# Kernel optimization log

Hardware: AMD Instinct MI355X
Metric: run time of the kernel (lower is better)

Reference implementation:

```python
import jax, jax.numpy as jnp
import numpy as np

M = 16            # num_frequencies
DIM = 512         # dim_input
B = 32768         # flattened batch
H = M + 1         # raw complex table side
N = 2 * M + 1     # autocorrelated table side
NPAR = H * H      # (m+1)^2


def setup_inputs() -> dict:
    key = jax.random.key(0)
    k1, k2, k3 = jax.random.split(key, 3)
    inputs = jax.random.normal(k1, (B, DIM), dtype=jnp.float32)
    targets = jax.random.uniform(k2, (B, 2), dtype=jnp.float32)  # points in [0,1) subset of [-1,1]^2
    # nn.init.normal_(weight, 0.01) => mean=0.01, std=1.0 ; bias zeros
    W = jax.random.normal(k3, (2 * NPAR, DIM), dtype=jnp.float32) + 0.01
    b = jnp.zeros((2 * NPAR,), dtype=jnp.float32)
    return {"inputs": inputs, "targets": targets, "W": W, "b": b}


def reference(inputs, targets, W, b):
    # Linear -> unconstrained complex (m+1)x(m+1) table per sample
    p = inputs @ W.T + b                                   # (B, 2*NPAR)
    real = p[:, :NPAR].reshape(-1, H, H)
    imag = p[:, NPAR:].reshape(-1, H, H)
    seq = jax.lax.complex(real, imag)                      # (B, H, H) complex64

    # 2D linear autocorrelation r[tau] = sum_i seq[i+tau] * conj(seq[i]),
    # tau in [-M, M]^2, via zero-padded FFT (equivalent to the grouped conv2d).
    F = jnp.fft.fft2(seq, s=(N, N))                        # (B, N, N)
    ac = jnp.fft.ifft2(F * jnp.conj(F))                    # circular autocorr
    ac = jnp.roll(ac, (M, M), axis=(-2, -1))               # index a -> lag a-M

    # Normalize so C[0,0] (= centre) equals 1/4 => unit mass on [-1,1]^2
    centre = ac[:, M, M].real                              # sum |seq|^2 > 0
    C = ac / (4.0 * centre)[:, None, None]                 # (B, N, N)

    # Evaluate f(x,y) = sum_{kx,ky} C * exp(i*pi*(kx*x + ky*y))
    k = jnp.arange(-M, M + 1, dtype=jnp.float32)
    kx, ky = jnp.meshgrid(k, k, indexing='xy')             # (N, N)
    tx = targets[:, 0][:, None, None]
    ty = targets[:, 1][:, None, None]
    phase = kx[None] * tx + ky[None] * ty                  # (B, N, N)
    exps = jnp.exp(1j * jnp.pi * phase)
    pdf = jnp.einsum('bij,bij->b', C, exps).real           # (B,)
    return pdf
```

## Files before the change

### kernel.cpp

```cpp
#include <hip/hip_runtime.h>

#define NPARC 289
#define NOUT  578
#define DIMK  512
#define CTILES 40
#define BATCH 32768

typedef __bf16 bf16x8 __attribute__((ext_vector_type(8)));
typedef float floatx4 __attribute__((ext_vector_type(4)));

__device__ __forceinline__ unsigned short f2bf(float f) {
    unsigned u = __float_as_uint(f);
    u = (u + 0x7fffu + ((u >> 16) & 1u)) >> 16;
    return (unsigned short)u;
}

__global__ void prep_w(const float* __restrict__ W, unsigned short* __restrict__ Wp) {
    int wid = threadIdx.x >> 6;
    int lane = threadIdx.x & 63;
    int col = blockIdx.x * 4 + wid;
    int k = lane * 8;
    unsigned short v[8];
    if (col < NOUT) {
        const float* src = W + (size_t)col * DIMK + k;
        #pragma unroll
        for (int j = 0; j < 8; ++j) v[j] = f2bf(src[j]);
    } else {
        #pragma unroll
        for (int j = 0; j < 8; ++j) v[j] = 0;
    }
    int ct = col >> 4;
    int ks = k >> 5;
    int ln = (((k >> 3) & 3) << 4) + (col & 15);
    uint4 o;
    o.x = (unsigned)v[0] | ((unsigned)v[1] << 16);
    o.y = (unsigned)v[2] | ((unsigned)v[3] << 16);
    o.z = (unsigned)v[4] | ((unsigned)v[5] << 16);
    o.w = (unsigned)v[6] | ((unsigned)v[7] << 16);
    *(uint4*)(Wp + (size_t)((ct * 16 + ks) * 64 + ln) * 8) = o;
}

__global__ __launch_bounds__(256, 2) void fused_kernel(
    const float* __restrict__ inputs, const float* __restrict__ targets,
    const float* __restrict__ bias, const unsigned short* __restrict__ Wp,
    float* __restrict__ out)
{
    __shared__ __align__(16) unsigned short Alds[64 * 64 * 8];
    const int tid = threadIdx.x;
    const int base = blockIdx.x * 64;

    const float4* inp4 = (const float4*)(inputs + (size_t)base * DIMK);
    #pragma unroll
    for (int i = 0; i < 32; ++i) {
        int f = i * 256 + tid;
        int s = f >> 7;
        int k = (f & 127) * 4;
        float4 v = inp4[f];
        int t = ((s >> 4) << 4) + (k >> 5);
        int ln = ((((k >> 3) & 3) << 4) + (s & 15)) ^ (t & 7);
        int off = (t * 64 + ln) * 8 + (k & 7);
        uint2 w;
        w.x = (unsigned)f2bf(v.x) | ((unsigned)f2bf(v.y) << 16);
        w.y = (unsigned)f2bf(v.z) | ((unsigned)f2bf(v.w) << 16);
        *(uint2*)&Alds[off] = w;
    }
    __syncthreads();

    const int wid  = tid >> 6;
    const int lane = tid & 63;
    const int quad = lane >> 4;
    const int lcol = lane & 15;

    float xs[4], ys[4];
    #pragma unroll
    for (int st = 0; st < 4; ++st) {
        float2 t2 = *(const float2*)(targets + 2 * (base + st * 16 + lcol));
        xs[st] = t2.x;
        ys[st] = t2.y;
    }

    float pd[4] = {0.f,0.f,0.f,0.f};
    float pr[4] = {0.f,0.f,0.f,0.f};
    float pim[4] = {0.f,0.f,0.f,0.f};

    const bf16x8* Wf = (const bf16x8*)Wp;

    #pragma unroll 1
    for (int pp = 0; pp < 5; ++pp) {
        const int wct0 = wid * 10 + pp * 2;
        floatx4 acc[2][4];
        #pragma unroll
        for (int w2 = 0; w2 < 2; ++w2)
            #pragma unroll
            for (int st = 0; st < 4; ++st) acc[w2][st] = (floatx4){0.f,0.f,0.f,0.f};

        const bf16x8* awp = Wf + ((size_t)(wct0 * 16) * 64 + lane);

        #pragma unroll 4
        for (int ks = 0; ks < 16; ++ks) {
            bf16x8 aw[2], bs[4];
            #pragma unroll
            for (int w2 = 0; w2 < 2; ++w2)
                aw[w2] = awp[(size_t)(w2 * 16 + ks) * 64];
            #pragma unroll
            for (int st = 0; st < 4; ++st) {
                int t = st * 16 + ks;
                bs[st] = *(const bf16x8*)&Alds[(t * 64 + (lane ^ (t & 7))) * 8];
            }
            #pragma unroll
            for (int w2 = 0; w2 < 2; ++w2)
                #pragma unroll
                for (int st = 0; st < 4; ++st)
                    acc[w2][st] = __builtin_amdgcn_mfma_f32_16x16x32_bf16(
                        aw[w2], bs[st], acc[w2][st], 0, 0, 0);
        }

        #pragma unroll
        for (int w2 = 0; w2 < 2; ++w2)
            #pragma unroll
            for (int reg = 0; reg < 4; ++reg) {
                int colw = (wct0 + w2) * 16 + quad * 4 + reg;
                if (colw < NOUT) {
                    bool im = (colw >= NPARC);
                    int idx = im ? colw - NPARC : colw;
                    int r = idx / 17;
                    int c = idx - r * 17;
                    float cf = (float)c, rf = (float)r;
                    float bb = bias[colw];
                    #pragma unroll
                    for (int st = 0; st < 4; ++st) {
                        float val = acc[w2][st][reg] + bb;
                        float phi = 3.14159265358979323846f * fmaf(cf, xs[st], rf * ys[st]);
                        float sn = __sinf(phi);
                        float cs = __cosf(phi);
                        float a1 = im ? -sn : cs;
                        float a2 = im ?  cs : sn;
                        pd[st]  = fmaf(val, val, pd[st]);
                        pr[st]  = fmaf(val, a1, pr[st]);
                        pim[st] = fmaf(val, a2, pim[st]);
                    }
                }
            }
    }

    #pragma unroll
    for (int d = 16; d < 64; d <<= 1)
        #pragma unroll
        for (int st = 0; st < 4; ++st) {
            pd[st]  += __shfl_xor(pd[st], d, 64);
            pr[st]  += __shfl_xor(pr[st], d, 64);
            pim[st] += __shfl_xor(pim[st], d, 64);
        }

    __syncthreads();
    float* R = (float*)Alds;
    if (lane < 16) {
        #pragma unroll
        for (int st = 0; st < 4; ++st) {
            int sl = st * 16 + lane;
            R[(wid * 64 + sl) * 3 + 0] = pd[st];
            R[(wid * 64 + sl) * 3 + 1] = pr[st];
            R[(wid * 64 + sl) * 3 + 2] = pim[st];
        }
    }
    __syncthreads();

    if (tid < 64) {
        float sd = 0.f, sr = 0.f, si = 0.f;
        #pragma unroll
        for (int w = 0; w < 4; ++w) {
            sd += R[(w * 64 + tid) * 3 + 0];
            sr += R[(w * 64 + tid) * 3 + 1];
            si += R[(w * 64 + tid) * 3 + 2];
        }
        out[base + tid] = (sr * sr + si * si) / (4.0f * sd);
    }
}

extern "C" void kernel_launch(void* const* d_in, const int* in_sizes, int n_in,
                              void* d_out, int out_size, void* d_ws, size_t ws_size,
                              hipStream_t stream) {
    const float* inputs  = (const float*)d_in[0];
    const float* targets = (const float*)d_in[1];
    const float* W       = (const float*)d_in[2];
    const float* bias    = (const float*)d_in[3];
    unsigned short* Wp   = (unsigned short*)d_ws;

    prep_w<<<CTILES * 16 / 4, 256, 0, stream>>>(W, Wp);
    fused_kernel<<<BATCH / 64, 256, 0, stream>>>(inputs, targets, bias, Wp, (float*)d_out);
}
```

Baseline: 123.0 us.

## Use 8 waves per block with single-pass GEMM and hardware sin/cos

```diff
diff --git a/kernel.cpp b/kernel.cpp
--- a/kernel.cpp
+++ b/kernel.cpp
@@ -40,7 +40,7 @@
     *(uint4*)(Wp + (size_t)((ct * 16 + ks) * 64 + ln) * 8) = o;
 }
 
-__global__ __launch_bounds__(256, 2) void fused_kernel(
+__global__ __launch_bounds__(512, 4) void fused_kernel(
     const float* __restrict__ inputs, const float* __restrict__ targets,
     const float* __restrict__ bias, const unsigned short* __restrict__ Wp,
     float* __restrict__ out)
@@ -51,18 +51,18 @@
 
     const float4* inp4 = (const float4*)(inputs + (size_t)base * DIMK);
     #pragma unroll
-    for (int i = 0; i < 32; ++i) {
-        int f = i * 256 + tid;
+    for (int i = 0; i < 16; ++i) {
+        int f = i * 512 + tid;
         int s = f >> 7;
         int k = (f & 127) * 4;
         float4 v = inp4[f];
         int t = ((s >> 4) << 4) + (k >> 5);
         int ln = ((((k >> 3) & 3) << 4) + (s & 15)) ^ (t & 7);
         int off = (t * 64 + ln) * 8 + (k & 7);
-        uint2 w;
-        w.x = (unsigned)f2bf(v.x) | ((unsigned)f2bf(v.y) << 16);
-        w.y = (unsigned)f2bf(v.z) | ((unsigned)f2bf(v.w) << 16);
-        *(uint2*)&Alds[off] = w;
+        union { __bf16 h[4]; uint2 u; } cv;
+        cv.h[0] = (__bf16)v.x; cv.h[1] = (__bf16)v.y;
+        cv.h[2] = (__bf16)v.z; cv.h[3] = (__bf16)v.w;
+        *(uint2*)&Alds[off] = cv.u;
     }
     __syncthreads();
 
@@ -71,77 +71,72 @@
     const int quad = lane >> 4;
     const int lcol = lane & 15;
 
+    floatx4 acc[5][4];
+    #pragma unroll
+    for (int t5 = 0; t5 < 5; ++t5)
+        #pragma unroll
+        for (int st = 0; st < 4; ++st) acc[t5][st] = (floatx4){0.f,0.f,0.f,0.f};
+
+    const bf16x8* Wf = (const bf16x8*)Wp;
+    const bf16x8* awp = Wf + ((size_t)(wid * 5 * 16) * 64 + lane);
+
+    #pragma unroll 1
+    for (int ks = 0; ks < 16; ++ks) {
+        bf16x8 bs[4];
+        #pragma unroll
+        for (int st = 0; st < 4; ++st) {
+            int t = st * 16 + ks;
+            bs[st] = *(const bf16x8*)&Alds[(t * 64 + (lane ^ (t & 7))) * 8];
+        }
+        #pragma unroll
+        for (int t5 = 0; t5 < 5; ++t5) {
+            bf16x8 aw = awp[(size_t)(t5 * 16 + ks) * 64];
+            #pragma unroll
+            for (int st = 0; st < 4; ++st)
+                acc[t5][st] = __builtin_amdgcn_mfma_f32_16x16x32_bf16(
+                    aw, bs[st], acc[t5][st], 0, 0, 0);
+        }
+    }
+
     float xs[4], ys[4];
     #pragma unroll
     for (int st = 0; st < 4; ++st) {
         float2 t2 = *(const float2*)(targets + 2 * (base + st * 16 + lcol));
-        xs[st] = t2.x;
-        ys[st] = t2.y;
+        xs[st] = 0.5f * t2.x;
+        ys[st] = 0.5f * t2.y;
     }
 
-    float pd[4] = {0.f,0.f,0.f,0.f};
-    float pr[4] = {0.f,0.f,0.f,0.f};
+    float pd[4]  = {0.f,0.f,0.f,0.f};
+    float pr[4]  = {0.f,0.f,0.f,0.f};
     float pim[4] = {0.f,0.f,0.f,0.f};
 
-    const bf16x8* Wf = (const bf16x8*)Wp;
-
-    #pragma unroll 1
-    for (int pp = 0; pp < 5; ++pp) {
-        const int wct0 = wid * 10 + pp * 2;
-        floatx4 acc[2][4];
+    #pragma unroll
+    for (int t5 = 0; t5 < 5; ++t5)
         #pragma unroll
-        for (int w2 = 0; w2 < 2; ++w2)
-            #pragma unroll
-            for (int st = 0; st < 4; ++st) acc[w2][st] = (floatx4){0.f,0.f,0.f,0.f};
-
-        const bf16x8* awp = Wf + ((size_t)(wct0 * 16) * 64 + lane);
-
-        #pragma unroll 4
-        for (int ks = 0; ks < 16; ++ks) {
-            bf16x8 aw[2], bs[4];
-            #pragma unroll
-            for (int w2 = 0; w2 < 2; ++w2)
-                aw[w2] = awp[(size_t)(w2 * 16 + ks) * 64];
-            #pragma unroll
-            for (int st = 0; st < 4; ++st) {
-                int t = st * 16 + ks;
-                bs[st] = *(const bf16x8*)&Alds[(t * 64 + (lane ^ (t & 7))) * 8];
-            }
-            #pragma unroll
-            for (int w2 = 0; w2 < 2; ++w2)
+        for (int reg = 0; reg < 4; ++reg) {
+            int colw = (wid * 5 + t5) * 16 + quad * 4 + reg;
+            if (colw < NOUT) {
+                bool im = (colw >= NPARC);
+                int idx = im ? colw - NPARC : colw;
+                int r = idx / 17;
+                int c = idx - r * 17;
+                float cf = (float)c, rf = (float)r;
+                float bb = bias[colw];
                 #pragma unroll
-                for (int st = 0; st < 4; ++st)
-                    acc[w2][st] = __builtin_amdgcn_mfma_f32_16x16x32_bf16(
-                        aw[w2], bs[st], acc[w2][st], 0, 0, 0);
-        }
-
-        #pragma unroll
-        for (int w2 = 0; w2 < 2; ++w2)
-            #pragma unroll
-            for (int reg = 0; reg < 4; ++reg) {
-                int colw = (wct0 + w2) * 16 + quad * 4 + reg;
-                if (colw < NOUT) {
-                    bool im = (colw >= NPARC);
-                    int idx = im ? colw - NPARC : colw;
-                    int r = idx / 17;
-                    int c = idx - r * 17;
-                    float cf = (float)c, rf = (float)r;
-                    float bb = bias[colw];
-                    #pragma unroll
-                    for (int st = 0; st < 4; ++st) {
-                        float val = acc[w2][st][reg] + bb;
-                        float phi = 3.14159265358979323846f * fmaf(cf, xs[st], rf * ys[st]);
-                        float sn = __sinf(phi);
-                        float cs = __cosf(phi);
-                        float a1 = im ? -sn : cs;
-                        float a2 = im ?  cs : sn;
-                        pd[st]  = fmaf(val, val, pd[st]);
-                        pr[st]  = fmaf(val, a1, pr[st]);
-                        pim[st] = fmaf(val, a2, pim[st]);
-                    }
+                for (int st = 0; st < 4; ++st) {
+                    float val = acc[t5][st][reg] + bb;
+                    float u = fmaf(cf, xs[st], rf * ys[st]);
+                    u = __builtin_amdgcn_fractf(u);
+                    float sn = __builtin_amdgcn_sinf(u);
+                    float cs = __builtin_amdgcn_cosf(u);
+                    float a1 = im ? -sn : cs;
+                    float a2 = im ?  cs : sn;
+                    pd[st]  = fmaf(val, val, pd[st]);
+                    pr[st]  = fmaf(val, a1, pr[st]);
+                    pim[st] = fmaf(val, a2, pim[st]);
                 }
             }
-    }
+        }
 
     #pragma unroll
     for (int d = 16; d < 64; d <<= 1)
@@ -168,7 +163,7 @@
     if (tid < 64) {
         float sd = 0.f, sr = 0.f, si = 0.f;
         #pragma unroll
-        for (int w = 0; w < 4; ++w) {
+        for (int w = 0; w < 8; ++w) {
             sd += R[(w * 64 + tid) * 3 + 0];
             sr += R[(w * 64 + tid) * 3 + 1];
             si += R[(w * 64 + tid) * 3 + 2];
@@ -187,5 +182,5 @@
     unsigned short* Wp   = (unsigned short*)d_ws;
 
     prep_w<<<CTILES * 16 / 4, 256, 0, stream>>>(W, Wp);
-    fused_kernel<<<BATCH / 64, 256, 0, stream>>>(inputs, targets, bias, Wp, (float*)d_out);
+    fused_kernel<<<BATCH / 64, 512, 0, stream>>>(inputs, targets, bias, Wp, (float*)d_out);
 }
```

After: 118.4 us. 3.7% less time.
